# Kernel tuning notes

Hardware: AMD Instinct MI355X
Metric: run time of the kernel (lower is better)

The kernel has to match this reference:

```python
import jax, jax.numpy as jnp
from jax import lax
import numpy as np

S, B, T = 512, 256, 128


def setup_inputs() -> dict:
    key = jax.random.key(0)
    k1, k2, k3, k4 = jax.random.split(key, 4)
    emissions = jax.random.normal(k1, (S, B, T), dtype=jnp.float32)
    mask = jnp.ones((S, B), dtype=jnp.int32)  # all positions valid
    start_transitions = jax.random.normal(k2, (T,), dtype=jnp.float32)
    end_transitions = jax.random.normal(k3, (T,), dtype=jnp.float32)
    transitions = jax.random.normal(k4, (T, T), dtype=jnp.float32)
    return {
        "emissions": emissions,
        "mask": mask,
        "start_transitions": start_transitions,
        "end_transitions": end_transitions,
        "transitions": transitions,
    }


def reference(emissions, mask, start_transitions, end_transitions, transitions):
    """Viterbi decode. emissions: [S,B,T], mask: [S,B].
    Returns (best_tags [B,S] int32, best_path_score [B] float32)."""
    seq_len, batch, num_tags = emissions.shape
    maskb = mask.astype(bool)

    score0 = start_transitions[None, :] + emissions[0]  # [B,T]

    def fwd_step(score, inp):
        em_t, m_t = inp  # [B,T], [B]
        # [B, T_prev, T_next]
        ns = score[:, :, None] + transitions[None, :, :] + em_t[:, None, :]
        next_score = ns.max(axis=1)          # [B,T]
        idx = ns.argmax(axis=1)              # [B,T] best previous tag
        score = jnp.where(m_t[:, None], next_score, score)
        return score, idx

    final_score, history = lax.scan(fwd_step, score0, (emissions[1:], maskb[1:]))
    final_score = final_score + end_transitions[None, :]

    best_last = jnp.argmax(final_score, axis=1)   # [B] tag at last valid position
    best_score = jnp.max(final_score, axis=1)     # [B]

    barange = jnp.arange(batch)

    def back_step(tag, inp):
        hist_t, m_t = inp  # [B,T], [B]
        prev = hist_t[barange, tag]
        tag = jnp.where(m_t, prev, tag)  # only follow history inside the sequence
        return tag, tag

    # reverse scan over transitions t -> t+1 for t = S-2 .. 0; ys[t] = tag at time t
    _, tags_prefix = lax.scan(back_step, best_last, (history, maskb[1:]), reverse=True)
    tags = jnp.concatenate([tags_prefix, best_last[None, :]], axis=0)  # [S,B]
    return tags.T.astype(jnp.int32), best_score
```

## Files before the change

### kernel.cpp

```cpp
#include <hip/hip_runtime.h>

#define SLEN  512
#define BATCH 256
#define NTAGS 128
#define NTHR  1024

__device__ __forceinline__ int dpp_qperm_b1(int x) {
    return __builtin_amdgcn_update_dpp(0, x, 0xB1, 0xF, 0xF, true);
}
__device__ __forceinline__ int dpp_qperm_4e(int x) {
    return __builtin_amdgcn_update_dpp(0, x, 0x4E, 0xF, 0xF, true);
}
__device__ __forceinline__ int swz_xor4(int x) {
    return __builtin_amdgcn_ds_swizzle(x, 0x101F);
}

struct VI { float v; int i; };
__device__ __forceinline__ VI vmax2(VI a, VI b) { return (b.v > a.v) ? b : a; }

__global__ __launch_bounds__(NTHR, 4) void viterbi_kernel(
    const float* __restrict__ em,
    const int*   __restrict__ mask,
    const float* __restrict__ start_t,
    const float* __restrict__ end_t,
    const float* __restrict__ trans,
    float* __restrict__ out)
{
    const int b    = blockIdx.x;
    const int tid  = threadIdx.x;
    const int j    = tid >> 3;
    const int h    = tid & 7;
    const int base = h << 4;
    const bool writer = (h == 0);
    const int jslot = j + (j >> 4) * 4;

    __shared__ __align__(16) float scbuf[2][8 * 20];
    __shared__ float fin[NTAGS];
    __shared__ int   maskv[SLEN];
    __shared__ unsigned char hist[SLEN - 1][NTAGS];
    __shared__ unsigned char exitc[8][NTAGS];
    __shared__ unsigned char st_tags[8];
    __shared__ unsigned char tagseq[SLEN];
    __shared__ float bestval_s;
    __shared__ int   bestj_s;

    const float* trp = trans + (size_t)base * NTAGS + j;
    const float t00 = trp[ 0*NTAGS], t01 = trp[ 1*NTAGS], t02 = trp[ 2*NTAGS], t03 = trp[ 3*NTAGS];
    const float t04 = trp[ 4*NTAGS], t05 = trp[ 5*NTAGS], t06 = trp[ 6*NTAGS], t07 = trp[ 7*NTAGS];
    const float t08 = trp[ 8*NTAGS], t09 = trp[ 9*NTAGS], t10 = trp[10*NTAGS], t11 = trp[11*NTAGS];
    const float t12 = trp[12*NTAGS], t13 = trp[13*NTAGS], t14 = trp[14*NTAGS], t15 = trp[15*NTAGS];

    if (tid < SLEN)
        maskv[tid] = mask[tid * BATCH + b];

    float scj = 0.f;
    if (writer) {
        scj = start_t[j] + em[(size_t)b * NTAGS + j];
        scbuf[0][jslot] = scj;
    }
    __syncthreads();

    const float* emp = em + (size_t)BATCH * NTAGS + (size_t)b * NTAGS + j;
    float em_next = *emp;

    int p = 0;
    for (int t = 1; t < SLEN; ++t) {
        const float em_cur = em_next;
        if (t + 1 < SLEN) { emp += BATCH * NTAGS; em_next = *emp; }

        const float4* sq = (const float4*)&scbuf[p][h * 20];
        const float4 q0 = sq[0], q1 = sq[1], q2 = sq[2], q3 = sq[3];

        const float c00 = (q0.x + t00) + em_cur, c01 = (q0.y + t01) + em_cur;
        const float c02 = (q0.z + t02) + em_cur, c03 = (q0.w + t03) + em_cur;
        const float c04 = (q1.x + t04) + em_cur, c05 = (q1.y + t05) + em_cur;
        const float c06 = (q1.z + t06) + em_cur, c07 = (q1.w + t07) + em_cur;
        const float c08 = (q2.x + t08) + em_cur, c09 = (q2.y + t09) + em_cur;
        const float c10 = (q2.z + t10) + em_cur, c11 = (q2.w + t11) + em_cur;
        const float c12 = (q3.x + t12) + em_cur, c13 = (q3.y + t13) + em_cur;
        const float c14 = (q3.z + t14) + em_cur, c15 = (q3.w + t15) + em_cur;

        const VI m0 = vmax2(VI{c00, 0}, VI{c01, 1}),  m1 = vmax2(VI{c02, 2}, VI{c03, 3});
        const VI m2 = vmax2(VI{c04, 4}, VI{c05, 5}),  m3 = vmax2(VI{c06, 6}, VI{c07, 7});
        const VI m4 = vmax2(VI{c08, 8}, VI{c09, 9}),  m5 = vmax2(VI{c10,10}, VI{c11,11});
        const VI m6 = vmax2(VI{c12,12}, VI{c13,13}),  m7 = vmax2(VI{c14,14}, VI{c15,15});
        const VI n0 = vmax2(m0, m1), n1 = vmax2(m2, m3);
        const VI n2 = vmax2(m4, m5), n3 = vmax2(m6, m7);
        const VI o0 = vmax2(n0, n1), o1 = vmax2(n2, n3);
        const VI r  = vmax2(o0, o1);

        float v  = r.v;
        int   gi = base + r.i;
        {
            float vo = __int_as_float(dpp_qperm_b1(__float_as_int(v)));
            int   io = dpp_qperm_b1(gi);
            if (vo > v) { v = vo; gi = io; }
        }
        {
            float vo = __int_as_float(dpp_qperm_4e(__float_as_int(v)));
            int   io = dpp_qperm_4e(gi);
            if (vo > v) { v = vo; gi = io; }
        }
        {
            float vo = __int_as_float(swz_xor4(__float_as_int(v)));
            int   io = swz_xor4(gi);
            if (vo > v) { v = vo; gi = io; }
        }

        if (writer) {
            hist[t - 1][j] = (unsigned char)gi;
            scj = maskv[t] ? v : scj;
            scbuf[p ^ 1][jslot] = scj;
        }
        __syncthreads();
        p ^= 1;
    }

    if (writer) fin[j] = scj + end_t[j];
    __syncthreads();

    if (tid < 64) {
        float v  = fin[tid]; int bj = tid;
        float v1 = fin[tid + 64];
        if (v1 > v) { v = v1; bj = tid + 64; }
#pragma unroll
        for (int off = 32; off > 0; off >>= 1) {
            float ov = __shfl_xor(v, off, 64);
            int   oj = __shfl_xor(bj, off, 64);
            if (ov > v || (ov == v && oj < bj)) { v = ov; bj = oj; }
        }
        if (tid == 0) { bestval_s = v; bestj_s = bj; }
    }
    __syncthreads();

    {
        const int k = tid & 127;
        const int c = tid >> 7;
        int tag = k;
        for (int u = 63; u >= 0; --u) {
            const int s = c * 64 + u;
            if (s <= SLEN - 2) {
                int pv = hist[s][tag];
                tag = maskv[s + 1] ? pv : tag;
            }
        }
        exitc[c][k] = (unsigned char)tag;
    }
    __syncthreads();

    if (tid == 0) {
        int tag = bestj_s;
        for (int c = 7; c >= 0; --c) {
            st_tags[c] = (unsigned char)tag;
            tag = exitc[c][tag];
        }
        out[BATCH * SLEN + b] = bestval_s;
    }
    __syncthreads();

    if (tid < 8) {
        const int c = tid;
        int tag = st_tags[c];
        if (c == 7) tagseq[SLEN - 1] = (unsigned char)tag;
        const int shi = (c == 7) ? (SLEN - 2) : (c * 64 + 63);
        for (int s = shi; s >= c * 64; --s) {
            int pv = hist[s][tag];
            tag = maskv[s + 1] ? pv : tag;
            tagseq[s] = (unsigned char)tag;
        }
    }
    __syncthreads();

    if (tid < SLEN)
        out[b * SLEN + tid] = (float)tagseq[tid];
}

extern "C" void kernel_launch(void* const* d_in, const int* in_sizes, int n_in,
                              void* d_out, int out_size, void* d_ws, size_t ws_size,
                              hipStream_t stream) {
    const float* em      = (const float*)d_in[0];
    const int*   mask    = (const int*)d_in[1];
    const float* start_t = (const float*)d_in[2];
    const float* end_t   = (const float*)d_in[3];
    const float* trans   = (const float*)d_in[4];
    float* out = (float*)d_out;

    viterbi_kernel<<<dim3(BATCH), dim3(NTHR), 0, stream>>>(
        em, mask, start_t, end_t, trans, out);
}
```

Baseline: 406.0 us.

## Specialize all-valid-mask path and replace syncthreads with raw LDS-only barrier

Detects in a block-wide pass whether every mask entry is valid and, if so, runs a copy of the forward loop with no per-step mask lookup. It also replaces __syncthreads with an inline s_waitcnt lgkmcnt(0) plus s_barrier, so the barrier waits only on LDS traffic and not on the outstanding global emission prefetch. An empty asm pins the transition values in vector registers. The raw barrier relies on the compiler not needing other fences, and the allv_s flag is set without any synchronisation between the writes.

Result: no change. 398.4 us (-1.9%).

```diff
diff --git a/kernel.cpp b/kernel.cpp
--- a/kernel.cpp
+++ b/kernel.cpp
@@ -17,6 +17,55 @@
 
 struct VI { float v; int i; };
 __device__ __forceinline__ VI vmax2(VI a, VI b) { return (b.v > a.v) ? b : a; }
+
+#define VIT_STEP(USE_MASK)                                                     \
+  {                                                                            \
+    const float em_cur = em_next;                                              \
+    if (t + 1 < SLEN) { emp += BATCH * NTAGS; em_next = *emp; }                \
+    const float4* sq = (const float4*)&scbuf[p][h * 20];                       \
+    const float4 q0 = sq[0], q1 = sq[1], q2 = sq[2], q3 = sq[3];               \
+    const float c00 = (q0.x + t00) + em_cur, c01 = (q0.y + t01) + em_cur;      \
+    const float c02 = (q0.z + t02) + em_cur, c03 = (q0.w + t03) + em_cur;      \
+    const float c04 = (q1.x + t04) + em_cur, c05 = (q1.y + t05) + em_cur;      \
+    const float c06 = (q1.z + t06) + em_cur, c07 = (q1.w + t07) + em_cur;      \
+    const float c08 = (q2.x + t08) + em_cur, c09 = (q2.y + t09) + em_cur;      \
+    const float c10 = (q2.z + t10) + em_cur, c11 = (q2.w + t11) + em_cur;      \
+    const float c12 = (q3.x + t12) + em_cur, c13 = (q3.y + t13) + em_cur;      \
+    const float c14 = (q3.z + t14) + em_cur, c15 = (q3.w + t15) + em_cur;      \
+    const VI m0 = vmax2(VI{c00, 0}, VI{c01, 1}),  m1 = vmax2(VI{c02, 2}, VI{c03, 3}); \
+    const VI m2 = vmax2(VI{c04, 4}, VI{c05, 5}),  m3 = vmax2(VI{c06, 6}, VI{c07, 7}); \
+    const VI m4 = vmax2(VI{c08, 8}, VI{c09, 9}),  m5 = vmax2(VI{c10,10}, VI{c11,11}); \
+    const VI m6 = vmax2(VI{c12,12}, VI{c13,13}),  m7 = vmax2(VI{c14,14}, VI{c15,15}); \
+    const VI n0 = vmax2(m0, m1), n1 = vmax2(m2, m3);                           \
+    const VI n2 = vmax2(m4, m5), n3 = vmax2(m6, m7);                           \
+    const VI o0 = vmax2(n0, n1), o1 = vmax2(n2, n3);                           \
+    const VI r  = vmax2(o0, o1);                                               \
+    float v  = r.v;                                                            \
+    int   gi = base + r.i;                                                     \
+    {                                                                          \
+      float vo = __int_as_float(dpp_qperm_b1(__float_as_int(v)));              \
+      int   io = dpp_qperm_b1(gi);                                             \
+      if (vo > v) { v = vo; gi = io; }                                         \
+    }                                                                          \
+    {                                                                          \
+      float vo = __int_as_float(dpp_qperm_4e(__float_as_int(v)));              \
+      int   io = dpp_qperm_4e(gi);                                             \
+      if (vo > v) { v = vo; gi = io; }                                         \
+    }                                                                          \
+    {                                                                          \
+      float vo = __int_as_float(swz_xor4(__float_as_int(v)));                  \
+      int   io = swz_xor4(gi);                                                 \
+      if (vo > v) { v = vo; gi = io; }                                         \
+    }                                                                          \
+    if (writer) {                                                              \
+      hist[t - 1][j] = (unsigned char)gi;                                      \
+      if (USE_MASK) { scj = maskv[t] ? v : scj; } else { scj = v; }            \
+      scbuf[p ^ 1][jslot] = scj;                                               \
+    }                                                                          \
+     \
+    asm volatile("s_waitcnt lgkmcnt(0)\n\ts_barrier" ::: "memory");            \
+    p ^= 1;                                                                    \
+  }
 
 __global__ __launch_bounds__(NTHR, 4) void viterbi_kernel(
     const float* __restrict__ em,
@@ -37,6 +86,7 @@
     __shared__ __align__(16) float scbuf[2][8 * 20];
     __shared__ float fin[NTAGS];
     __shared__ int   maskv[SLEN];
+    __shared__ int   allv_s;
     __shared__ unsigned char hist[SLEN - 1][NTAGS];
     __shared__ unsigned char exitc[8][NTAGS];
     __shared__ unsigned char st_tags[8];
@@ -45,13 +95,23 @@
     __shared__ int   bestj_s;
 
     const float* trp = trans + (size_t)base * NTAGS + j;
-    const float t00 = trp[ 0*NTAGS], t01 = trp[ 1*NTAGS], t02 = trp[ 2*NTAGS], t03 = trp[ 3*NTAGS];
-    const float t04 = trp[ 4*NTAGS], t05 = trp[ 5*NTAGS], t06 = trp[ 6*NTAGS], t07 = trp[ 7*NTAGS];
-    const float t08 = trp[ 8*NTAGS], t09 = trp[ 9*NTAGS], t10 = trp[10*NTAGS], t11 = trp[11*NTAGS];
-    const float t12 = trp[12*NTAGS], t13 = trp[13*NTAGS], t14 = trp[14*NTAGS], t15 = trp[15*NTAGS];
-
-    if (tid < SLEN)
-        maskv[tid] = mask[tid * BATCH + b];
+    float t00 = trp[ 0*NTAGS], t01 = trp[ 1*NTAGS], t02 = trp[ 2*NTAGS], t03 = trp[ 3*NTAGS];
+    float t04 = trp[ 4*NTAGS], t05 = trp[ 5*NTAGS], t06 = trp[ 6*NTAGS], t07 = trp[ 7*NTAGS];
+    float t08 = trp[ 8*NTAGS], t09 = trp[ 9*NTAGS], t10 = trp[10*NTAGS], t11 = trp[11*NTAGS];
+    float t12 = trp[12*NTAGS], t13 = trp[13*NTAGS], t14 = trp[14*NTAGS], t15 = trp[15*NTAGS];
+    asm volatile("" : "+v"(t00), "+v"(t01), "+v"(t02), "+v"(t03),
+                      "+v"(t04), "+v"(t05), "+v"(t06), "+v"(t07),
+                      "+v"(t08), "+v"(t09), "+v"(t10), "+v"(t11),
+                      "+v"(t12), "+v"(t13), "+v"(t14), "+v"(t15));
+
+    if (tid == 0) allv_s = 1;
+    int mv = 1;
+    if (tid < SLEN) {
+        mv = mask[tid * BATCH + b];
+        maskv[tid] = mv;
+    }
+    __syncthreads();
+    if (mv == 0) allv_s = 0;
 
     float scj = 0.f;
     if (writer) {
@@ -59,61 +119,16 @@
         scbuf[0][jslot] = scj;
     }
     __syncthreads();
+    const int allv = allv_s;
 
     const float* emp = em + (size_t)BATCH * NTAGS + (size_t)b * NTAGS + j;
     float em_next = *emp;
 
     int p = 0;
-    for (int t = 1; t < SLEN; ++t) {
-        const float em_cur = em_next;
-        if (t + 1 < SLEN) { emp += BATCH * NTAGS; em_next = *emp; }
-
-        const float4* sq = (const float4*)&scbuf[p][h * 20];
-        const float4 q0 = sq[0], q1 = sq[1], q2 = sq[2], q3 = sq[3];
-
-        const float c00 = (q0.x + t00) + em_cur, c01 = (q0.y + t01) + em_cur;
-        const float c02 = (q0.z + t02) + em_cur, c03 = (q0.w + t03) + em_cur;
-        const float c04 = (q1.x + t04) + em_cur, c05 = (q1.y + t05) + em_cur;
-        const float c06 = (q1.z + t06) + em_cur, c07 = (q1.w + t07) + em_cur;
-        const float c08 = (q2.x + t08) + em_cur, c09 = (q2.y + t09) + em_cur;
-        const float c10 = (q2.z + t10) + em_cur, c11 = (q2.w + t11) + em_cur;
-        const float c12 = (q3.x + t12) + em_cur, c13 = (q3.y + t13) + em_cur;
-        const float c14 = (q3.z + t14) + em_cur, c15 = (q3.w + t15) + em_cur;
-
-        const VI m0 = vmax2(VI{c00, 0}, VI{c01, 1}),  m1 = vmax2(VI{c02, 2}, VI{c03, 3});
-        const VI m2 = vmax2(VI{c04, 4}, VI{c05, 5}),  m3 = vmax2(VI{c06, 6}, VI{c07, 7});
-        const VI m4 = vmax2(VI{c08, 8}, VI{c09, 9}),  m5 = vmax2(VI{c10,10}, VI{c11,11});
-        const VI m6 = vmax2(VI{c12,12}, VI{c13,13}),  m7 = vmax2(VI{c14,14}, VI{c15,15});
-        const VI n0 = vmax2(m0, m1), n1 = vmax2(m2, m3);
-        const VI n2 = vmax2(m4, m5), n3 = vmax2(m6, m7);
-        const VI o0 = vmax2(n0, n1), o1 = vmax2(n2, n3);
-        const VI r  = vmax2(o0, o1);
-
-        float v  = r.v;
-        int   gi = base + r.i;
-        {
-            float vo = __int_as_float(dpp_qperm_b1(__float_as_int(v)));
-            int   io = dpp_qperm_b1(gi);
-            if (vo > v) { v = vo; gi = io; }
-        }
-        {
-            float vo = __int_as_float(dpp_qperm_4e(__float_as_int(v)));
-            int   io = dpp_qperm_4e(gi);
-            if (vo > v) { v = vo; gi = io; }
-        }
-        {
-            float vo = __int_as_float(swz_xor4(__float_as_int(v)));
-            int   io = swz_xor4(gi);
-            if (vo > v) { v = vo; gi = io; }
-        }
-
-        if (writer) {
-            hist[t - 1][j] = (unsigned char)gi;
-            scj = maskv[t] ? v : scj;
-            scbuf[p ^ 1][jslot] = scj;
-        }
-        __syncthreads();
-        p ^= 1;
+    if (allv) {
+        for (int t = 1; t < SLEN; ++t) VIT_STEP(0)
+    } else {
+        for (int t = 1; t < SLEN; ++t) VIT_STEP(1)
     }
 
     if (writer) fin[j] = scj + end_t[j];
```

## Give each thread two output tags and use DPP row shifts for reduction

Applied to the files above, without the earlier changes.

Each step of the forward pass is re-split. A thread now scores two adjacent next-tags over 8 previous tags (16 lanes per tag pair) instead of one next-tag over 16 previous tags (8 lanes per tag). The cross-lane argmax now runs entirely through DPP: two quad permutes followed by row_shl 4 and row_shl 8, replacing the ds_swizzle step. Only lane 0 of each row holds the correct result, which suffices because only the writer lane uses it. The aim is to cut LDS swizzle latency and score-buffer reads on the serial per-step critical path and gain ILP from two independent reduction chains, at the cost of an extra reduction level and more VGPR pressure.

Measured after the change: 467.9 us. +15.2%, slower.

```diff
diff --git a/kernel.cpp b/kernel.cpp
--- a/kernel.cpp
+++ b/kernel.cpp
@@ -11,12 +11,38 @@
 __device__ __forceinline__ int dpp_qperm_4e(int x) {
     return __builtin_amdgcn_update_dpp(0, x, 0x4E, 0xF, 0xF, true);
 }
-__device__ __forceinline__ int swz_xor4(int x) {
-    return __builtin_amdgcn_ds_swizzle(x, 0x101F);
+__device__ __forceinline__ int dpp_row_shl4(int x) {
+    return __builtin_amdgcn_update_dpp(0, x, 0x104, 0xF, 0xF, true);
+}
+__device__ __forceinline__ int dpp_row_shl8(int x) {
+    return __builtin_amdgcn_update_dpp(0, x, 0x108, 0xF, 0xF, true);
 }
 
 struct VI { float v; int i; };
 __device__ __forceinline__ VI vmax2(VI a, VI b) { return (b.v > a.v) ? b : a; }
+
+__device__ __forceinline__ void bfly16(float& v, int& gi) {
+    {
+        float vo = __int_as_float(dpp_qperm_b1(__float_as_int(v)));
+        int   io = dpp_qperm_b1(gi);
+        if (vo > v) { v = vo; gi = io; }
+    }
+    {
+        float vo = __int_as_float(dpp_qperm_4e(__float_as_int(v)));
+        int   io = dpp_qperm_4e(gi);
+        if (vo > v) { v = vo; gi = io; }
+    }
+    {
+        float vo = __int_as_float(dpp_row_shl4(__float_as_int(v)));
+        int   io = dpp_row_shl4(gi);
+        if (vo > v) { v = vo; gi = io; }
+    }
+    {
+        float vo = __int_as_float(dpp_row_shl8(__float_as_int(v)));
+        int   io = dpp_row_shl8(gi);
+        if (vo > v) { v = vo; gi = io; }
+    }
+}
 
 __global__ __launch_bounds__(NTHR, 4) void viterbi_kernel(
     const float* __restrict__ em,
@@ -28,13 +54,14 @@
 {
     const int b    = blockIdx.x;
     const int tid  = threadIdx.x;
-    const int j    = tid >> 3;
-    const int h    = tid & 7;
-    const int base = h << 4;
+    const int jp   = tid >> 4;
+    const int j1   = jp << 1;
+    const int h    = tid & 15;
+    const int base = h << 3;
     const bool writer = (h == 0);
-    const int jslot = j + (j >> 4) * 4;
-
-    __shared__ __align__(16) float scbuf[2][8 * 20];
+    const int jslot = (j1 >> 3) * 12 + (j1 & 7);
+
+    __shared__ __align__(16) float scbuf[2][16 * 12];
     __shared__ float fin[NTAGS];
     __shared__ int   maskv[SLEN];
     __shared__ unsigned char hist[SLEN - 1][NTAGS];
@@ -44,79 +71,88 @@
     __shared__ float bestval_s;
     __shared__ int   bestj_s;
 
-    const float* trp = trans + (size_t)base * NTAGS + j;
-    const float t00 = trp[ 0*NTAGS], t01 = trp[ 1*NTAGS], t02 = trp[ 2*NTAGS], t03 = trp[ 3*NTAGS];
-    const float t04 = trp[ 4*NTAGS], t05 = trp[ 5*NTAGS], t06 = trp[ 6*NTAGS], t07 = trp[ 7*NTAGS];
-    const float t08 = trp[ 8*NTAGS], t09 = trp[ 9*NTAGS], t10 = trp[10*NTAGS], t11 = trp[11*NTAGS];
-    const float t12 = trp[12*NTAGS], t13 = trp[13*NTAGS], t14 = trp[14*NTAGS], t15 = trp[15*NTAGS];
+    const float* trp = trans + (size_t)base * NTAGS + j1;
+    const float2 w0 = *(const float2*)(trp + 0 * NTAGS);
+    const float2 w1 = *(const float2*)(trp + 1 * NTAGS);
+    const float2 w2 = *(const float2*)(trp + 2 * NTAGS);
+    const float2 w3 = *(const float2*)(trp + 3 * NTAGS);
+    const float2 w4 = *(const float2*)(trp + 4 * NTAGS);
+    const float2 w5 = *(const float2*)(trp + 5 * NTAGS);
+    const float2 w6 = *(const float2*)(trp + 6 * NTAGS);
+    const float2 w7 = *(const float2*)(trp + 7 * NTAGS);
+    const float ta0 = w0.x, tb0 = w0.y, ta1 = w1.x, tb1 = w1.y;
+    const float ta2 = w2.x, tb2 = w2.y, ta3 = w3.x, tb3 = w3.y;
+    const float ta4 = w4.x, tb4 = w4.y, ta5 = w5.x, tb5 = w5.y;
+    const float ta6 = w6.x, tb6 = w6.y, ta7 = w7.x, tb7 = w7.y;
 
     if (tid < SLEN)
         maskv[tid] = mask[tid * BATCH + b];
 
-    float scj = 0.f;
+    float scjA = 0.f, scjB = 0.f;
     if (writer) {
-        scj = start_t[j] + em[(size_t)b * NTAGS + j];
-        scbuf[0][jslot] = scj;
-    }
-    __syncthreads();
-
-    const float* emp = em + (size_t)BATCH * NTAGS + (size_t)b * NTAGS + j;
-    float em_next = *emp;
+        scjA = start_t[j1]     + em[(size_t)b * NTAGS + j1];
+        scjB = start_t[j1 + 1] + em[(size_t)b * NTAGS + j1 + 1];
+        scbuf[0][jslot]     = scjA;
+        scbuf[0][jslot + 1] = scjB;
+    }
+    __syncthreads();
+
+    const float2* emp2 = (const float2*)(em + (size_t)BATCH * NTAGS
+                                            + (size_t)b * NTAGS + j1);
+    float2 em_next = *emp2;
 
     int p = 0;
     for (int t = 1; t < SLEN; ++t) {
-        const float em_cur = em_next;
-        if (t + 1 < SLEN) { emp += BATCH * NTAGS; em_next = *emp; }
-
-        const float4* sq = (const float4*)&scbuf[p][h * 20];
-        const float4 q0 = sq[0], q1 = sq[1], q2 = sq[2], q3 = sq[3];
-
-        const float c00 = (q0.x + t00) + em_cur, c01 = (q0.y + t01) + em_cur;
-        const float c02 = (q0.z + t02) + em_cur, c03 = (q0.w + t03) + em_cur;
-        const float c04 = (q1.x + t04) + em_cur, c05 = (q1.y + t05) + em_cur;
-        const float c06 = (q1.z + t06) + em_cur, c07 = (q1.w + t07) + em_cur;
-        const float c08 = (q2.x + t08) + em_cur, c09 = (q2.y + t09) + em_cur;
-        const float c10 = (q2.z + t10) + em_cur, c11 = (q2.w + t11) + em_cur;
-        const float c12 = (q3.x + t12) + em_cur, c13 = (q3.y + t13) + em_cur;
-        const float c14 = (q3.z + t14) + em_cur, c15 = (q3.w + t15) + em_cur;
-
-        const VI m0 = vmax2(VI{c00, 0}, VI{c01, 1}),  m1 = vmax2(VI{c02, 2}, VI{c03, 3});
-        const VI m2 = vmax2(VI{c04, 4}, VI{c05, 5}),  m3 = vmax2(VI{c06, 6}, VI{c07, 7});
-        const VI m4 = vmax2(VI{c08, 8}, VI{c09, 9}),  m5 = vmax2(VI{c10,10}, VI{c11,11});
-        const VI m6 = vmax2(VI{c12,12}, VI{c13,13}),  m7 = vmax2(VI{c14,14}, VI{c15,15});
-        const VI n0 = vmax2(m0, m1), n1 = vmax2(m2, m3);
-        const VI n2 = vmax2(m4, m5), n3 = vmax2(m6, m7);
-        const VI o0 = vmax2(n0, n1), o1 = vmax2(n2, n3);
-        const VI r  = vmax2(o0, o1);
-
-        float v  = r.v;
-        int   gi = base + r.i;
-        {
-            float vo = __int_as_float(dpp_qperm_b1(__float_as_int(v)));
-            int   io = dpp_qperm_b1(gi);
-            if (vo > v) { v = vo; gi = io; }
-        }
-        {
-            float vo = __int_as_float(dpp_qperm_4e(__float_as_int(v)));
-            int   io = dpp_qperm_4e(gi);
-            if (vo > v) { v = vo; gi = io; }
-        }
-        {
-            float vo = __int_as_float(swz_xor4(__float_as_int(v)));
-            int   io = swz_xor4(gi);
-            if (vo > v) { v = vo; gi = io; }
-        }
+        const float emA = em_next.x, emB = em_next.y;
+        if (t + 1 < SLEN) { emp2 += (BATCH * NTAGS) / 2; em_next = *emp2; }
+
+        const float4* sq = (const float4*)&scbuf[p][h * 12];
+        const float4 q0 = sq[0], q1 = sq[1];
+
+        const float ac0 = (q0.x + ta0) + emA, ac1 = (q0.y + ta1) + emA;
+        const float ac2 = (q0.z + ta2) + emA, ac3 = (q0.w + ta3) + emA;
+        const float ac4 = (q1.x + ta4) + emA, ac5 = (q1.y + ta5) + emA;
+        const float ac6 = (q1.z + ta6) + emA, ac7 = (q1.w + ta7) + emA;
+        const VI am0 = vmax2(VI{ac0, 0}, VI{ac1, 1});
+        const VI am1 = vmax2(VI{ac2, 2}, VI{ac3, 3});
+        const VI am2 = vmax2(VI{ac4, 4}, VI{ac5, 5});
+        const VI am3 = vmax2(VI{ac6, 6}, VI{ac7, 7});
+        const VI an0 = vmax2(am0, am1), an1 = vmax2(am2, am3);
+        const VI ar  = vmax2(an0, an1);
+
+        const float bc0 = (q0.x + tb0) + emB, bc1 = (q0.y + tb1) + emB;
+        const float bc2 = (q0.z + tb2) + emB, bc3 = (q0.w + tb3) + emB;
+        const float bc4 = (q1.x + tb4) + emB, bc5 = (q1.y + tb5) + emB;
+        const float bc6 = (q1.z + tb6) + emB, bc7 = (q1.w + tb7) + emB;
+        const VI bm0 = vmax2(VI{bc0, 0}, VI{bc1, 1});
+        const VI bm1 = vmax2(VI{bc2, 2}, VI{bc3, 3});
+        const VI bm2 = vmax2(VI{bc4, 4}, VI{bc5, 5});
+        const VI bm3 = vmax2(VI{bc6, 6}, VI{bc7, 7});
+        const VI bn0 = vmax2(bm0, bm1), bn1 = vmax2(bm2, bm3);
+        const VI br  = vmax2(bn0, bn1);
+
+        float vA = ar.v;  int giA = base + ar.i;
+        float vB = br.v;  int giB = base + br.i;
+        bfly16(vA, giA);
+        bfly16(vB, giB);
 
         if (writer) {
-            hist[t - 1][j] = (unsigned char)gi;
-            scj = maskv[t] ? v : scj;
-            scbuf[p ^ 1][jslot] = scj;
+            hist[t - 1][j1]     = (unsigned char)giA;
+            hist[t - 1][j1 + 1] = (unsigned char)giB;
+            const int mm = maskv[t];
+            scjA = mm ? vA : scjA;
+            scjB = mm ? vB : scjB;
+            scbuf[p ^ 1][jslot]     = scjA;
+            scbuf[p ^ 1][jslot + 1] = scjB;
         }
         __syncthreads();
         p ^= 1;
     }
 
-    if (writer) fin[j] = scj + end_t[j];
+    if (writer) {
+        fin[j1]     = scjA + end_t[j1];
+        fin[j1 + 1] = scjB + end_t[j1 + 1];
+    }
     __syncthreads();
 
     if (tid < 64) {
```

## Halve block size, give each thread two output tags per Viterbi step

Applied to the files above, without the earlier changes.

The block shrinks from 1024 to 512 threads. Each 8-lane group now computes two next-tag maxima, reusing the same shared-memory score loads, with float2 loads for transitions and emissions. The per-step __syncthreads is replaced by an inline s_waitcnt plus s_barrier, and the backtrace chunking is reworked so each thread walks two chunks. This cuts the number of waves that take part in each per-step barrier and amortizes the LDS reads, in exchange for more work and registers per thread.

New measurement: 411.5 us. About the same (+1.3%).

```diff
diff --git a/kernel.cpp b/kernel.cpp
--- a/kernel.cpp
+++ b/kernel.cpp
@@ -3,7 +3,7 @@
 #define SLEN  512
 #define BATCH 256
 #define NTAGS 128
-#define NTHR  1024
+#define NTHR  512
 
 __device__ __forceinline__ int dpp_qperm_b1(int x) {
     return __builtin_amdgcn_update_dpp(0, x, 0xB1, 0xF, 0xF, true);
@@ -18,7 +18,25 @@
 struct VI { float v; int i; };
 __device__ __forceinline__ VI vmax2(VI a, VI b) { return (b.v > a.v) ? b : a; }
 
-__global__ __launch_bounds__(NTHR, 4) void viterbi_kernel(
+__device__ __forceinline__ void bfly8(float& v, int& gi) {
+    {
+        float vo = __int_as_float(dpp_qperm_b1(__float_as_int(v)));
+        int   io = dpp_qperm_b1(gi);
+        if (vo > v) { v = vo; gi = io; }
+    }
+    {
+        float vo = __int_as_float(dpp_qperm_4e(__float_as_int(v)));
+        int   io = dpp_qperm_4e(gi);
+        if (vo > v) { v = vo; gi = io; }
+    }
+    {
+        float vo = __int_as_float(swz_xor4(__float_as_int(v)));
+        int   io = swz_xor4(gi);
+        if (vo > v) { v = vo; gi = io; }
+    }
+}
+
+__global__ __launch_bounds__(NTHR, 2) void viterbi_kernel(
     const float* __restrict__ em,
     const int*   __restrict__ mask,
     const float* __restrict__ start_t,
@@ -28,11 +46,12 @@
 {
     const int b    = blockIdx.x;
     const int tid  = threadIdx.x;
-    const int j    = tid >> 3;
+    const int jp   = tid >> 3;
+    const int j1   = jp << 1;
     const int h    = tid & 7;
     const int base = h << 4;
     const bool writer = (h == 0);
-    const int jslot = j + (j >> 4) * 4;
+    const int jslot = j1 + ((j1 >> 4) << 2);
 
     __shared__ __align__(16) float scbuf[2][8 * 20];
     __shared__ float fin[NTAGS];
@@ -44,79 +63,104 @@
     __shared__ float bestval_s;
     __shared__ int   bestj_s;
 
-    const float* trp = trans + (size_t)base * NTAGS + j;
-    const float t00 = trp[ 0*NTAGS], t01 = trp[ 1*NTAGS], t02 = trp[ 2*NTAGS], t03 = trp[ 3*NTAGS];
-    const float t04 = trp[ 4*NTAGS], t05 = trp[ 5*NTAGS], t06 = trp[ 6*NTAGS], t07 = trp[ 7*NTAGS];
-    const float t08 = trp[ 8*NTAGS], t09 = trp[ 9*NTAGS], t10 = trp[10*NTAGS], t11 = trp[11*NTAGS];
-    const float t12 = trp[12*NTAGS], t13 = trp[13*NTAGS], t14 = trp[14*NTAGS], t15 = trp[15*NTAGS];
+    const float* trp = trans + (size_t)base * NTAGS + j1;
+    const float2 w00 = *(const float2*)(trp +  0*NTAGS), w01 = *(const float2*)(trp +  1*NTAGS);
+    const float2 w02 = *(const float2*)(trp +  2*NTAGS), w03 = *(const float2*)(trp +  3*NTAGS);
+    const float2 w04 = *(const float2*)(trp +  4*NTAGS), w05 = *(const float2*)(trp +  5*NTAGS);
+    const float2 w06 = *(const float2*)(trp +  6*NTAGS), w07 = *(const float2*)(trp +  7*NTAGS);
+    const float2 w08 = *(const float2*)(trp +  8*NTAGS), w09 = *(const float2*)(trp +  9*NTAGS);
+    const float2 w10 = *(const float2*)(trp + 10*NTAGS), w11 = *(const float2*)(trp + 11*NTAGS);
+    const float2 w12 = *(const float2*)(trp + 12*NTAGS), w13 = *(const float2*)(trp + 13*NTAGS);
+    const float2 w14 = *(const float2*)(trp + 14*NTAGS), w15 = *(const float2*)(trp + 15*NTAGS);
+    const float ta00 = w00.x, tb00 = w00.y, ta01 = w01.x, tb01 = w01.y;
+    const float ta02 = w02.x, tb02 = w02.y, ta03 = w03.x, tb03 = w03.y;
+    const float ta04 = w04.x, tb04 = w04.y, ta05 = w05.x, tb05 = w05.y;
+    const float ta06 = w06.x, tb06 = w06.y, ta07 = w07.x, tb07 = w07.y;
+    const float ta08 = w08.x, tb08 = w08.y, ta09 = w09.x, tb09 = w09.y;
+    const float ta10 = w10.x, tb10 = w10.y, ta11 = w11.x, tb11 = w11.y;
+    const float ta12 = w12.x, tb12 = w12.y, ta13 = w13.x, tb13 = w13.y;
+    const float ta14 = w14.x, tb14 = w14.y, ta15 = w15.x, tb15 = w15.y;
 
     if (tid < SLEN)
         maskv[tid] = mask[tid * BATCH + b];
 
-    float scj = 0.f;
+    float scjA = 0.f, scjB = 0.f;
     if (writer) {
-        scj = start_t[j] + em[(size_t)b * NTAGS + j];
-        scbuf[0][jslot] = scj;
-    }
-    __syncthreads();
-
-    const float* emp = em + (size_t)BATCH * NTAGS + (size_t)b * NTAGS + j;
-    float em_next = *emp;
+        scjA = start_t[j1]     + em[(size_t)b * NTAGS + j1];
+        scjB = start_t[j1 + 1] + em[(size_t)b * NTAGS + j1 + 1];
+        scbuf[0][jslot]     = scjA;
+        scbuf[0][jslot + 1] = scjB;
+    }
+    __syncthreads();
+
+    const float2* emp2 = (const float2*)(em + (size_t)BATCH * NTAGS
+                                            + (size_t)b * NTAGS + j1);
+    float2 em_next = *emp2;
 
     int p = 0;
     for (int t = 1; t < SLEN; ++t) {
-        const float em_cur = em_next;
-        if (t + 1 < SLEN) { emp += BATCH * NTAGS; em_next = *emp; }
+        const float emA = em_next.x, emB = em_next.y;
+        if (t + 1 < SLEN) { emp2 += (BATCH * NTAGS) / 2; em_next = *emp2; }
 
         const float4* sq = (const float4*)&scbuf[p][h * 20];
         const float4 q0 = sq[0], q1 = sq[1], q2 = sq[2], q3 = sq[3];
 
-        const float c00 = (q0.x + t00) + em_cur, c01 = (q0.y + t01) + em_cur;
-        const float c02 = (q0.z + t02) + em_cur, c03 = (q0.w + t03) + em_cur;
-        const float c04 = (q1.x + t04) + em_cur, c05 = (q1.y + t05) + em_cur;
-        const float c06 = (q1.z + t06) + em_cur, c07 = (q1.w + t07) + em_cur;
-        const float c08 = (q2.x + t08) + em_cur, c09 = (q2.y + t09) + em_cur;
-        const float c10 = (q2.z + t10) + em_cur, c11 = (q2.w + t11) + em_cur;
-        const float c12 = (q3.x + t12) + em_cur, c13 = (q3.y + t13) + em_cur;
-        const float c14 = (q3.z + t14) + em_cur, c15 = (q3.w + t15) + em_cur;
-
-        const VI m0 = vmax2(VI{c00, 0}, VI{c01, 1}),  m1 = vmax2(VI{c02, 2}, VI{c03, 3});
-        const VI m2 = vmax2(VI{c04, 4}, VI{c05, 5}),  m3 = vmax2(VI{c06, 6}, VI{c07, 7});
-        const VI m4 = vmax2(VI{c08, 8}, VI{c09, 9}),  m5 = vmax2(VI{c10,10}, VI{c11,11});
-        const VI m6 = vmax2(VI{c12,12}, VI{c13,13}),  m7 = vmax2(VI{c14,14}, VI{c15,15});
-        const VI n0 = vmax2(m0, m1), n1 = vmax2(m2, m3);
-        const VI n2 = vmax2(m4, m5), n3 = vmax2(m6, m7);
-        const VI o0 = vmax2(n0, n1), o1 = vmax2(n2, n3);
-        const VI r  = vmax2(o0, o1);
-
-        float v  = r.v;
-        int   gi = base + r.i;
-        {
-            float vo = __int_as_float(dpp_qperm_b1(__float_as_int(v)));
-            int   io = dpp_qperm_b1(gi);
-            if (vo > v) { v = vo; gi = io; }
-        }
-        {
-            float vo = __int_as_float(dpp_qperm_4e(__float_as_int(v)));
-            int   io = dpp_qperm_4e(gi);
-            if (vo > v) { v = vo; gi = io; }
-        }
-        {
-            float vo = __int_as_float(swz_xor4(__float_as_int(v)));
-            int   io = swz_xor4(gi);
-            if (vo > v) { v = vo; gi = io; }
-        }
+        const float a00 = (q0.x + ta00) + emA, a01 = (q0.y + ta01) + emA;
+        const float a02 = (q0.z + ta02) + emA, a03 = (q0.w + ta03) + emA;
+        const float a04 = (q1.x + ta04) + emA, a05 = (q1.y + ta05) + emA;
+        const float a06 = (q1.z + ta06) + emA, a07 = (q1.w + ta07) + emA;
+        const float a08 = (q2.x + ta08) + emA, a09 = (q2.y + ta09) + emA;
+        const float a10 = (q2.z + ta10) + emA, a11 = (q2.w + ta11) + emA;
+        const float a12 = (q3.x + ta12) + emA, a13 = (q3.y + ta13) + emA;
+        const float a14 = (q3.z + ta14) + emA, a15 = (q3.w + ta15) + emA;
+        const VI Am0 = vmax2(VI{a00, 0}, VI{a01, 1}),  Am1 = vmax2(VI{a02, 2}, VI{a03, 3});
+        const VI Am2 = vmax2(VI{a04, 4}, VI{a05, 5}),  Am3 = vmax2(VI{a06, 6}, VI{a07, 7});
+        const VI Am4 = vmax2(VI{a08, 8}, VI{a09, 9}),  Am5 = vmax2(VI{a10,10}, VI{a11,11});
+        const VI Am6 = vmax2(VI{a12,12}, VI{a13,13}),  Am7 = vmax2(VI{a14,14}, VI{a15,15});
+        const VI An0 = vmax2(Am0, Am1), An1 = vmax2(Am2, Am3);
+        const VI An2 = vmax2(Am4, Am5), An3 = vmax2(Am6, Am7);
+        const VI Ao0 = vmax2(An0, An1), Ao1 = vmax2(An2, An3);
+        const VI Ar  = vmax2(Ao0, Ao1);
+
+        const float b00 = (q0.x + tb00) + emB, b01 = (q0.y + tb01) + emB;
+        const float b02 = (q0.z + tb02) + emB, b03 = (q0.w + tb03) + emB;
+        const float b04 = (q1.x + tb04) + emB, b05 = (q1.y + tb05) + emB;
+        const float b06 = (q1.z + tb06) + emB, b07 = (q1.w + tb07) + emB;
+        const float b08 = (q2.x + tb08) + emB, b09 = (q2.y + tb09) + emB;
+        const float b10 = (q2.z + tb10) + emB, b11 = (q2.w + tb11) + emB;
+        const float b12 = (q3.x + tb12) + emB, b13 = (q3.y + tb13) + emB;
+        const float b14 = (q3.z + tb14) + emB, b15 = (q3.w + tb15) + emB;
+        const VI Bm0 = vmax2(VI{b00, 0}, VI{b01, 1}),  Bm1 = vmax2(VI{b02, 2}, VI{b03, 3});
+        const VI Bm2 = vmax2(VI{b04, 4}, VI{b05, 5}),  Bm3 = vmax2(VI{b06, 6}, VI{b07, 7});
+        const VI Bm4 = vmax2(VI{b08, 8}, VI{b09, 9}),  Bm5 = vmax2(VI{b10,10}, VI{b11,11});
+        const VI Bm6 = vmax2(VI{b12,12}, VI{b13,13}),  Bm7 = vmax2(VI{b14,14}, VI{b15,15});
+        const VI Bn0 = vmax2(Bm0, Bm1), Bn1 = vmax2(Bm2, Bm3);
+        const VI Bn2 = vmax2(Bm4, Bm5), Bn3 = vmax2(Bm6, Bm7);
+        const VI Bo0 = vmax2(Bn0, Bn1), Bo1 = vmax2(Bn2, Bn3);
+        const VI Br  = vmax2(Bo0, Bo1);
+
+        float vA = Ar.v;  int giA = base + Ar.i;
+        float vB = Br.v;  int giB = base + Br.i;
+        bfly8(vA, giA);
+        bfly8(vB, giB);
 
         if (writer) {
-            hist[t - 1][j] = (unsigned char)gi;
-            scj = maskv[t] ? v : scj;
-            scbuf[p ^ 1][jslot] = scj;
-        }
-        __syncthreads();
+            hist[t - 1][j1]     = (unsigned char)giA;
+            hist[t - 1][j1 + 1] = (unsigned char)giB;
+            const int mm = maskv[t];
+            scjA = mm ? vA : scjA;
+            scjB = mm ? vB : scjB;
+            scbuf[p ^ 1][jslot]     = scjA;
+            scbuf[p ^ 1][jslot + 1] = scjB;
+        }
+        asm volatile("s_waitcnt lgkmcnt(0)\n\ts_barrier" ::: "memory");
         p ^= 1;
     }
 
-    if (writer) fin[j] = scj + end_t[j];
+    if (writer) {
+        fin[j1]     = scjA + end_t[j1];
+        fin[j1 + 1] = scjB + end_t[j1 + 1];
+    }
     __syncthreads();
 
     if (tid < 64) {
@@ -134,17 +178,22 @@
     __syncthreads();
 
     {
-        const int k = tid & 127;
-        const int c = tid >> 7;
-        int tag = k;
+        const int k  = tid & 127;
+        const int c0 = tid >> 7;
+        const int c1 = c0 + 4;
+        int tagA = k, tagB = k;
         for (int u = 63; u >= 0; --u) {
-            const int s = c * 64 + u;
-            if (s <= SLEN - 2) {
-                int pv = hist[s][tag];
-                tag = maskv[s + 1] ? pv : tag;
+            const int sA = c0 * 64 + u;
+            const int sB = c1 * 64 + u;
+            if (sB <= SLEN - 2) {
+                int pv = hist[sB][tagB];
+                tagB = maskv[sB + 1] ? pv : tagB;
             }
-        }
-        exitc[c][k] = (unsigned char)tag;
+            int pv = hist[sA][tagA];
+            tagA = maskv[sA + 1] ? pv : tagA;
+        }
+        exitc[c0][k] = (unsigned char)tagA;
+        exitc[c1][k] = (unsigned char)tagB;
     }
     __syncthreads();
 
@@ -171,8 +220,7 @@
     }
     __syncthreads();
 
-    if (tid < SLEN)
-        out[b * SLEN + tid] = (float)tagseq[tid];
+    out[b * SLEN + tid] = (float)tagseq[tid];
 }
 
 extern "C" void kernel_launch(void* const* d_in, const int* in_sizes, int n_in,
```
